# Kernel optimization log

Measured on AMD Instinct MI355X. Metric: run time of the kernel, lower is better.

The kernel has to match this reference:

```python
import jax, jax.numpy as jnp
import numpy as np

N = 50000
E = 800000
IN_C = 128
HID = 128
OUT_C = 64
HEADS = 8
HD1 = HID // HEADS   # 16 per-head dim, layer 1 (concat)
HD2 = OUT_C          # 64 per-head dim, layer 2 (concat=False, mean over heads)
NEG_SLOPE = 0.2


def setup_inputs() -> dict:
    key = jax.random.key(0)
    ks = jax.random.split(key, 12)
    x = jax.random.normal(ks[0], (N, IN_C), dtype=jnp.float32)
    edge_index = jax.random.randint(ks[1], (2, E), 0, N, dtype=jnp.int64)
    s1 = 1.0 / np.sqrt(IN_C)
    s2 = 1.0 / np.sqrt(HID)
    W1 = jax.random.normal(ks[2], (IN_C, HEADS * HD1), dtype=jnp.float32) * s1
    att_src1 = jax.random.normal(ks[3], (HEADS, HD1), dtype=jnp.float32) * s1
    att_dst1 = jax.random.normal(ks[4], (HEADS, HD1), dtype=jnp.float32) * s1
    b1 = jnp.zeros((HID,), dtype=jnp.float32)
    W2 = jax.random.normal(ks[5], (HID, HEADS * HD2), dtype=jnp.float32) * s2
    att_src2 = jax.random.normal(ks[6], (HEADS, HD2), dtype=jnp.float32) * s2
    att_dst2 = jax.random.normal(ks[7], (HEADS, HD2), dtype=jnp.float32) * s2
    b2 = jnp.zeros((OUT_C,), dtype=jnp.float32)
    return {"x": x, "edge_index": edge_index,
            "W1": W1, "att_src1": att_src1, "att_dst1": att_dst1, "b1": b1,
            "W2": W2, "att_src2": att_src2, "att_dst2": att_dst2, "b2": b2}


def _gat_conv(x, W, a_src, a_dst, bias, src, dst, heads, head_dim, concat):
    n = x.shape[0]
    h = (x @ W).reshape(n, heads, head_dim)                      # [N,H,D]
    alpha_s = jnp.einsum('nhd,hd->nh', h, a_src)                  # [N,H]
    alpha_d = jnp.einsum('nhd,hd->nh', h, a_dst)                  # [N,H]
    e = jax.nn.leaky_relu(alpha_s[src] + alpha_d[dst], NEG_SLOPE)  # [E,H]
    # segment softmax over edges grouped by destination node
    m = jax.ops.segment_max(e, dst, num_segments=n)               # [N,H]
    m = jnp.where(jnp.isfinite(m), m, 0.0)
    ex = jnp.exp(e - m[dst])
    denom = jax.ops.segment_sum(ex, dst, num_segments=n)
    alpha = ex / (denom[dst] + 1e-16)                             # [E,H]
    out = jax.ops.segment_sum(h[src] * alpha[:, :, None], dst, num_segments=n)  # [N,H,D]
    if concat:
        out = out.reshape(n, heads * head_dim)
    else:
        out = out.mean(axis=1)
    return out + bias


def reference(x, edge_index, W1, att_src1, att_dst1, b1, W2, att_src2, att_dst2, b2):
    # PyG GATConv default add_self_loops=True
    loops = jnp.arange(N, dtype=edge_index.dtype)
    src = jnp.concatenate([edge_index[0], loops])
    dst = jnp.concatenate([edge_index[1], loops])
    h = _gat_conv(x, W1, att_src1, att_dst1, b1, src, dst, HEADS, HD1, True)
    h = jax.nn.relu(h)
    out = _gat_conv(h, W2, att_src2, att_dst2, b2, src, dst, HEADS, HD2, False)
    return out
```

## Files before the change

kernel.cpp:

```cpp
#include <hip/hip_runtime.h>

#define N_NODES 50000
#define N_EDGES 800000
#define ET (N_EDGES + N_NODES)
#define HEADS 8
#define NPAD 50048
#define SCAN_NB 196
#define CAP 96

typedef __attribute__((ext_vector_type(8))) _Float16 half8;
typedef __attribute__((ext_vector_type(2))) _Float16 half2v;
typedef __attribute__((ext_vector_type(4))) float f32x4;

__device__ __forceinline__ int edge_src(const int* ei, int e, int is64){
  if (e >= N_EDGES) return e - N_EDGES;
  return is64 ? ei[2*e] : ei[e];
}
__device__ __forceinline__ int edge_dst(const int* ei, int e, int is64){
  if (e >= N_EDGES) return e - N_EDGES;
  return is64 ? ei[2*(N_EDGES + e)] : ei[N_EDGES + e];
}

__global__ void k_init(const int* __restrict__ ei, int* __restrict__ deg,
                       int* __restrict__ cnt, int* __restrict__ flag){
  int i = blockIdx.x*blockDim.x + threadIdx.x;
  if (i < N_NODES){ deg[i] = 0; cnt[i] = 0; }
  if (i == 0){
    int zeros = 0;
    for (int k = 0; k < 64; k++){
      if (ei[2*k + 1] == 0) zeros++;
    }
    *flag = (zeros >= 60) ? 1 : 0;
  }
}

__global__ void k_degree(const int* __restrict__ ei, int* __restrict__ deg,
                         const int* __restrict__ flag){
  int e = blockIdx.x*blockDim.x + threadIdx.x;
  if (e >= ET) return;
  int is64 = *flag;
  int d = edge_dst(ei, e, is64);
  atomicAdd(&deg[d], 1);
}

__global__ void k_scan_part(const int* __restrict__ deg, int* __restrict__ loc,
                            int* __restrict__ part){
  __shared__ int lds[256];
  int t = threadIdx.x, i = blockIdx.x*256 + t;
  int v = (i < N_NODES) ? deg[i] : 0;
  lds[t] = v;
  __syncthreads();
  for (int off = 1; off < 256; off <<= 1){
    int x = (t >= off) ? lds[t - off] : 0;
    __syncthreads();
    lds[t] += x;
    __syncthreads();
  }
  if (i < N_NODES) loc[i] = lds[t] - v;
  if (t == 255) part[blockIdx.x] = lds[255];
}

__global__ void k_scan_carry(int* __restrict__ part, int* __restrict__ carry){
  __shared__ int lds[256];
  int t = threadIdx.x;
  int v = (t < SCAN_NB) ? part[t] : 0;
  lds[t] = v;
  __syncthreads();
  for (int off = 1; off < 256; off <<= 1){
    int x = (t >= off) ? lds[t - off] : 0;
    __syncthreads();
    lds[t] += x;
    __syncthreads();
  }
  if (t < SCAN_NB) carry[t] = lds[t] - v;
}

__global__ void k_scan_add(const int* __restrict__ loc, const int* __restrict__ carry,
                           int* __restrict__ row_ptr){
  int i = blockIdx.x*blockDim.x + threadIdx.x;
  if (i < N_NODES) row_ptr[i] = loc[i] + carry[i >> 8];
  if (i == 0) row_ptr[N_NODES] = ET;
}

__global__ void k_fill(const int* __restrict__ ei, const int* __restrict__ row_ptr,
                       int* __restrict__ cnt, int* __restrict__ col,
                       const int* __restrict__ flag){
  int e = blockIdx.x*blockDim.x + threadIdx.x;
  if (e >= ET) return;
  int is64 = *flag;
  int s = edge_src(ei, e, is64);
  int d = edge_dst(ei, e, is64);
  int pos = atomicAdd(&cnt[d], 1);
  col[row_ptr[d] + pos] = s;
}

__global__ void k_wprep(const float* __restrict__ W1, const float* __restrict__ W2,
                        const float* __restrict__ as2, const float* __restrict__ ad2,
                        _Float16* __restrict__ Bp1, _Float16* __restrict__ Bp,
                        float* __restrict__ ws2, float* __restrict__ wd2){
  int b = blockIdx.x;
  int t_ = threadIdx.x;
  if (b < 256){
    int t = b*256 + t_;
    int j = t & 7, lane = (t >> 3) & 63, nt = (t >> 9) & 3, kt = t >> 11;
    int k = kt*32 + (lane >> 4)*8 + j;
    int c = nt*16 + (lane & 15);
    int h = k >> 7, kk = k & 127;
    Bp[t] = (_Float16)(0.125f * W2[kk*512 + h*64 + c]);
  } else if (b < 320){
    int t = (b - 256)*256 + t_;
    int j = t & 7, lane = (t >> 3) & 63, nt = (t >> 9) & 7, kt = t >> 12;
    int k = kt*32 + (lane >> 4)*8 + j;
    int c = nt*16 + (lane & 15);
    Bp1[t] = (_Float16)W1[k*128 + c];
  } else {
    int t = (b - 320)*256 + t_;
    int k = t >> 3, h = t & 7;
    float s = 0.f, d = 0.f;
    for (int dd = 0; dd < 64; dd++){
      float w = W2[k*512 + h*64 + dd];
      s += w * as2[h*64 + dd];
      d += w * ad2[h*64 + dd];
    }
    ws2[h*128 + k] = s;
    wd2[h*128 + k] = d;
  }
}

__global__ void __launch_bounds__(256) k_gemm1_mfma(
    const float* __restrict__ x, const _Float16* __restrict__ Bp1,
    _Float16* __restrict__ h1){
  int tid = threadIdx.x;
  int lane = tid & 63, wv = tid >> 6;
  int n0 = blockIdx.x*64 + wv*16;
  int rowA = n0 + (lane & 15);
  int koff = (lane >> 4)*8;
  const float* xr = x + (size_t)rowA*128 + koff;
  f32x4 acc[8];
  #pragma unroll
  for (int i = 0; i < 8; i++) acc[i] = (f32x4){0.f,0.f,0.f,0.f};
  bool inb = (rowA < N_NODES);
  #pragma unroll
  for (int kt = 0; kt < 4; kt++){
    half8 af;
    if (inb){
      float4 a0 = *(const float4*)(xr + kt*32);
      float4 a1 = *(const float4*)(xr + kt*32 + 4);
      af = (half8){(_Float16)a0.x,(_Float16)a0.y,(_Float16)a0.z,(_Float16)a0.w,
                   (_Float16)a1.x,(_Float16)a1.y,(_Float16)a1.z,(_Float16)a1.w};
    } else {
      af = (half8){0,0,0,0,0,0,0,0};
    }
    #pragma unroll
    for (int nt = 0; nt < 8; nt++){
      half8 bf = *(const half8*)(Bp1 + (((kt*8 + nt)*64 + lane) << 3));
      acc[nt] = __builtin_amdgcn_mfma_f32_16x16x32_f16(af, bf, acc[nt], 0, 0, 0);
    }
  }
  int r0 = n0 + (lane >> 4)*4;
  #pragma unroll
  for (int nt = 0; nt < 8; nt++){
    int c = nt*16 + (lane & 15);
    #pragma unroll
    for (int r = 0; r < 4; r++){
      int n = r0 + r;
      if (n < N_NODES) h1[(size_t)n*128 + c] = (_Float16)acc[nt][r];
    }
  }
}

__global__ void k_alpha1(const _Float16* __restrict__ h1, const float* __restrict__ as1,
                         const float* __restrict__ ad1,
                         float* __restrict__ als, float* __restrict__ ald){
  int t = blockIdx.x*blockDim.x + threadIdx.x;
  if (t >= N_NODES*8) return;
  int n = t >> 3, hh = t & 7;
  const half2v* hp = (const half2v*)(h1 + (size_t)n*128 + hh*16);
  float s = 0.f, d = 0.f;
  #pragma unroll
  for (int i = 0; i < 8; i++){
    half2v v = hp[i];
    float vx = (float)v.x, vy = (float)v.y;
    s += vx*as1[hh*16 + 2*i] + vy*as1[hh*16 + 2*i + 1];
    d += vx*ad1[hh*16 + 2*i] + vy*ad1[hh*16 + 2*i + 1];
  }
  als[t] = s; ald[t] = d;
}

__global__ void k_attn_agg1(const _Float16* __restrict__ h1,
    const float* __restrict__ als, const float* __restrict__ ald,
    const int* __restrict__ row_ptr, const int* __restrict__ col,
    const float* __restrict__ bias, _Float16* __restrict__ hr,
    const float* __restrict__ ws2, const float* __restrict__ wd2,
    float* __restrict__ als2, float* __restrict__ ald2){
  __shared__ _Float16 ew_s[4][CAP*8];
  __shared__ int col_s[4][CAP];
  int tid = threadIdx.x;
  int wv = tid >> 6, lane = tid & 63;
  int n = blockIdx.x*4 + wv;
  int beg = row_ptr[n], end = row_ptr[n+1];
  int deg = end - beg;
  int items = deg*8;
  int h = lane & 7;
  float ad = ald[n*8 + h];
  _Float16* es = ew_s[wv];
  int* cs = col_s[wv];
  float l = 0.f;
  for (int it = lane; it < items; it += 64){
    int e = it >> 3;
    int s = col[beg + e];
    float a = als[s*8 + h] + ad;
    a = (a > 0.f) ? a : 0.2f*a;
    float ex = __expf(a);
    if (it < CAP*8){
      es[it] = (_Float16)ex;
      if ((it & 7) == 0) cs[e] = s;
    }
    l += ex;
  }
  l += __shfl_xor(l, 8, 64);
  l += __shfl_xor(l, 16, 64);
  l += __shfl_xor(l, 32, 64);
  float inv = 1.f / (l + 1e-16f);
  __syncthreads();
  int hh0 = lane >> 3;
  float invh = __shfl(inv, hh0, 64);
  const half2v* h2p = (const half2v*)h1;
  float ax = 0.f, ay = 0.f;
  int degc = deg < CAP ? deg : CAP;
  int j = 0;
  for (; j + 3 < degc; j += 4){
    int s0 = cs[j], s1 = cs[j+1], s2 = cs[j+2], s3 = cs[j+3];
    float w0 = (float)es[j*8 + hh0]     * invh;
    float w1 = (float)es[(j+1)*8 + hh0] * invh;
    float w2 = (float)es[(j+2)*8 + hh0] * invh;
    float w3 = (float)es[(j+3)*8 + hh0] * invh;
    half2v v0 = h2p[(size_t)s0*64 + lane];
    half2v v1 = h2p[(size_t)s1*64 + lane];
    half2v v2 = h2p[(size_t)s2*64 + lane];
    half2v v3 = h2p[(size_t)s3*64 + lane];
    ax += w0*(float)v0.x + w1*(float)v1.x + w2*(float)v2.x + w3*(float)v3.x;
    ay += w0*(float)v0.y + w1*(float)v1.y + w2*(float)v2.y + w3*(float)v3.y;
  }
  for (; j < degc; j++){
    int s = cs[j];
    float w = (float)es[j*8 + hh0] * invh;
    half2v v = h2p[(size_t)s*64 + lane];
    ax += w*(float)v.x; ay += w*(float)v.y;
  }
  float adh = ald[n*8 + hh0];
  for (; j < deg; j++){
    int s = col[beg + j];
    float a = als[s*8 + hh0] + adh;
    a = (a > 0.f) ? a : 0.2f*a;
    float w = __expf(a)*invh;
    half2v v = h2p[(size_t)s*64 + lane];
    ax += w*(float)v.x; ay += w*(float)v.y;
  }
  float2 bb = ((const float2*)bias)[lane];
  float o0 = fmaxf(ax + bb.x, 0.f);
  float o1 = fmaxf(ay + bb.y, 0.f);
  half2v oo; oo.x = (_Float16)o0; oo.y = (_Float16)o1;
  ((half2v*)hr)[(size_t)n*64 + lane] = oo;
  const float2* wsp = (const float2*)ws2;
  const float2* wdp = (const float2*)wd2;
  #pragma unroll
  for (int hh = 0; hh < 8; hh++){
    float2 a = wsp[hh*64 + lane];
    float2 b = wdp[hh*64 + lane];
    float vs = o0*a.x + o1*a.y;
    float vd = o0*b.x + o1*b.y;
    #pragma unroll
    for (int off = 1; off < 64; off <<= 1){
      vs += __shfl_xor(vs, off, 64);
      vd += __shfl_xor(vd, off, 64);
    }
    if (lane == 0){
      als2[n*8 + hh] = vs;
      ald2[n*8 + hh] = vd;
    }
  }
}

__global__ void k_attn_agg2(const _Float16* __restrict__ hr,
    const float* __restrict__ als, const float* __restrict__ ald,
    const int* __restrict__ row_ptr, const int* __restrict__ col,
    _Float16* __restrict__ aggb){
  __shared__ _Float16 ew_s[4][CAP*8];
  __shared__ int col_s[4][CAP];
  int tid = threadIdx.x;
  int wv = tid >> 6, lane = tid & 63;
  int n = blockIdx.x*4 + wv;
  int beg = row_ptr[n], end = row_ptr[n+1];
  int deg = end - beg;
  int items = deg*8;
  int h = lane & 7;
  float ad = ald[n*8 + h];
  _Float16* es = ew_s[wv];
  int* cs = col_s[wv];
  float l = 0.f;
  for (int it = lane; it < items; it += 64){
    int e = it >> 3;
    int s = col[beg + e];
    float a = als[s*8 + h] + ad;
    a = (a > 0.f) ? a : 0.2f*a;
    float ex = __expf(a);
    if (it < CAP*8){
      es[it] = (_Float16)ex;
      if ((it & 7) == 0) cs[e] = s;
    }
    l += ex;
  }
  l += __shfl_xor(l, 8, 64);
  l += __shfl_xor(l, 16, 64);
  l += __shfl_xor(l, 32, 64);
  float inv = 1.f / (l + 1e-16f);
  __syncthreads();
  int hq = lane & 7, gq = lane >> 3;
  _Float16 inv16 = (_Float16)inv;
  half2v acc[8];
  #pragma unroll
  for (int i = 0; i < 8; i++) acc[i] = (half2v){(_Float16)0.f, (_Float16)0.f};
  int degc = deg < CAP ? deg : CAP;
  int j = 0;
  for (; j + 3 < degc; j += 4){
    int s0 = cs[j], s1 = cs[j+1], s2 = cs[j+2], s3 = cs[j+3];
    _Float16 w0 = es[j*8 + hq]     * inv16;
    _Float16 w1 = es[(j+1)*8 + hq] * inv16;
    _Float16 w2 = es[(j+2)*8 + hq] * inv16;
    _Float16 w3 = es[(j+3)*8 + hq] * inv16;
    half2v w0p = {w0, w0}, w1p = {w1, w1}, w2p = {w2, w2}, w3p = {w3, w3};
    const _Float16* p0 = hr + (size_t)s0*128 + gq*16;
    const _Float16* p1 = hr + (size_t)s1*128 + gq*16;
    const _Float16* p2 = hr + (size_t)s2*128 + gq*16;
    const _Float16* p3 = hr + (size_t)s3*128 + gq*16;
    half8 va0 = *(const half8*)p0, vb0 = *(const half8*)(p0 + 8);
    half8 va1 = *(const half8*)p1, vb1 = *(const half8*)(p1 + 8);
    half8 va2 = *(const half8*)p2, vb2 = *(const half8*)(p2 + 8);
    half8 va3 = *(const half8*)p3, vb3 = *(const half8*)(p3 + 8);
    #pragma unroll
    for (int k = 0; k < 4; k++){
      acc[k]   += w0p * (half2v){va0[2*k], va0[2*k+1]};
      acc[k+4] += w0p * (half2v){vb0[2*k], vb0[2*k+1]};
      acc[k]   += w1p * (half2v){va1[2*k], va1[2*k+1]};
      acc[k+4] += w1p * (half2v){vb1[2*k], vb1[2*k+1]};
      acc[k]   += w2p * (half2v){va2[2*k], va2[2*k+1]};
      acc[k+4] += w2p * (half2v){vb2[2*k], vb2[2*k+1]};
      acc[k]   += w3p * (half2v){va3[2*k], va3[2*k+1]};
      acc[k+4] += w3p * (half2v){vb3[2*k], vb3[2*k+1]};
    }
  }
  for (; j < degc; j++){
    int s = cs[j];
    _Float16 wh = es[j*8 + hq] * inv16;
    half2v wp = {wh, wh};
    const _Float16* p = hr + (size_t)s*128 + gq*16;
    half8 va = *(const half8*)p, vb = *(const half8*)(p + 8);
    #pragma unroll
    for (int k = 0; k < 4; k++){
      acc[k]   += wp * (half2v){va[2*k], va[2*k+1]};
      acc[k+4] += wp * (half2v){vb[2*k], vb[2*k+1]};
    }
  }
  for (; j < deg; j++){
    int s = col[beg + j];
    float a = als[s*8 + hq] + ad;
    a = (a > 0.f) ? a : 0.2f*a;
    _Float16 wh = (_Float16)(__expf(a)*inv);
    half2v wp = {wh, wh};
    const _Float16* p = hr + (size_t)s*128 + gq*16;
    half8 va = *(const half8*)p, vb = *(const half8*)(p + 8);
    #pragma unroll
    for (int k = 0; k < 4; k++){
      acc[k]   += wp * (half2v){va[2*k], va[2*k+1]};
      acc[k+4] += wp * (half2v){vb[2*k], vb[2*k+1]};
    }
  }
  _Float16* ar = aggb + (size_t)n*1024 + hq*128 + gq*16;
  half8 oa, ob;
  #pragma unroll
  for (int k = 0; k < 4; k++){
    oa[2*k] = acc[k].x;   oa[2*k+1] = acc[k].y;
    ob[2*k] = acc[k+4].x; ob[2*k+1] = acc[k+4].y;
  }
  *(half8*)ar = oa;
  *(half8*)(ar + 8) = ob;
}

__global__ void __launch_bounds__(256) k_gemm_out_mfma(
    const _Float16* __restrict__ aggb, const _Float16* __restrict__ Bp,
    const float* __restrict__ b2, float* __restrict__ outp){
  int tid = threadIdx.x;
  int lane = tid & 63, wv = tid >> 6;
  int n0 = blockIdx.x*64 + wv*16;
  int rowA = n0 + (lane & 15);
  const _Float16* arow = aggb + (size_t)rowA*1024 + (lane >> 4)*8;
  f32x4 acc[4];
  #pragma unroll
  for (int i = 0; i < 4; i++) acc[i] = (f32x4){0.f,0.f,0.f,0.f};
  half8 af = *(const half8*)(arow);
  for (int kt = 0; kt < 32; kt++){
    half8 afn;
    if (kt + 1 < 32) afn = *(const half8*)(arow + (kt+1)*32);
    #pragma unroll
    for (int nt = 0; nt < 4; nt++){
      half8 bf = *(const half8*)(Bp + (((kt*4 + nt)*64 + lane) << 3));
      acc[nt] = __builtin_amdgcn_mfma_f32_16x16x32_f16(af, bf, acc[nt], 0, 0, 0);
    }
    af = afn;
  }
  int r0 = n0 + (lane >> 4)*4;
  #pragma unroll
  for (int nt = 0; nt < 4; nt++){
    int c = nt*16 + (lane & 15);
    float bb = b2[c];
    #pragma unroll
    for (int r = 0; r < 4; r++){
      int n = r0 + r;
      if (n < N_NODES) outp[n*64 + c] = acc[nt][r] + bb;
    }
  }
}

extern "C" void kernel_launch(void* const* d_in, const int* in_sizes, int n_in,
                              void* d_out, int out_size, void* d_ws, size_t ws_size,
                              hipStream_t stream){
  const float* x   = (const float*)d_in[0];
  const int*   ei  = (const int*)d_in[1];
  const float* W1  = (const float*)d_in[2];
  const float* as1 = (const float*)d_in[3];
  const float* ad1 = (const float*)d_in[4];
  const float* b1  = (const float*)d_in[5];
  const float* W2  = (const float*)d_in[6];
  const float* as2 = (const float*)d_in[7];
  const float* ad2 = (const float*)d_in[8];
  const float* b2  = (const float*)d_in[9];
  float* outp = (float*)d_out;

  char* p = (char*)d_ws;
  auto alloc = [&](size_t bytes) -> void* {
    void* r = (void*)p;
    p += (bytes + 255) & ~(size_t)255;
    return r;
  };
  _Float16* aggb = (_Float16*)alloc((size_t)NPAD*1024*2);
  _Float16* h1  = aggb;
  _Float16* hr  = (_Float16*)alloc((size_t)N_NODES*128*2);
  float* als1 = (float*)alloc((size_t)N_NODES*8*4);
  float* ald1 = (float*)alloc((size_t)N_NODES*8*4);
  float* als2 = (float*)alloc((size_t)N_NODES*8*4);
  float* ald2 = (float*)alloc((size_t)N_NODES*8*4);
  int* row_ptr = (int*)alloc((size_t)(N_NODES+1)*4);
  int* deg  = (int*)alloc((size_t)N_NODES*4);
  int* cnt  = (int*)alloc((size_t)N_NODES*4);
  int* col  = (int*)alloc((size_t)ET*4);
  int* loc  = (int*)alloc((size_t)N_NODES*4);
  int* part = (int*)alloc(256*4);
  int* carry= (int*)alloc(256*4);
  int* flag = (int*)alloc(256);
  float* ws2 = (float*)alloc(1024*4);
  float* wd2 = (float*)alloc(1024*4);
  _Float16* Bp1 = (_Float16*)alloc((size_t)16384*2);
  _Float16* Bp  = (_Float16*)alloc((size_t)65536*2);

  dim3 b256(256);
  k_init<<<(N_NODES+255)/256, b256, 0, stream>>>(ei, deg, cnt, flag);
  k_degree<<<(ET+255)/256, b256, 0, stream>>>(ei, deg, flag);
  k_scan_part<<<SCAN_NB, b256, 0, stream>>>(deg, loc, part);
  k_scan_carry<<<1, b256, 0, stream>>>(part, carry);
  k_scan_add<<<SCAN_NB, b256, 0, stream>>>(loc, carry, row_ptr);
  k_fill<<<(ET+255)/256, b256, 0, stream>>>(ei, row_ptr, cnt, col, flag);
  k_wprep<<<324, b256, 0, stream>>>(W1, W2, as2, ad2, Bp1, Bp, ws2, wd2);

  int nnode_blocks = N_NODES/4;
  int nh_blocks = (N_NODES*8 + 255)/256;
  k_gemm1_mfma<<<NPAD/64, b256, 0, stream>>>(x, Bp1, h1);
  k_alpha1<<<nh_blocks, b256, 0, stream>>>(h1, as1, ad1, als1, ald1);
  k_attn_agg1<<<nnode_blocks, b256, 0, stream>>>(h1, als1, ald1, row_ptr, col,
                                                 b1, hr, ws2, wd2, als2, ald2);
  k_attn_agg2<<<nnode_blocks, b256, 0, stream>>>(hr, als2, ald2, row_ptr, col, aggb);
  k_gemm_out_mfma<<<NPAD/64, b256, 0, stream>>>(aggb, Bp, b2, outp);
}
```

Baseline: 384.6 us.

## Fuse alpha1 into GEMM1 epilogue and restructure layer-2 score reduction

```diff
diff --git a/kernel.cpp b/kernel.cpp
--- a/kernel.cpp
+++ b/kernel.cpp
@@ -129,7 +129,9 @@
 
 __global__ void __launch_bounds__(256) k_gemm1_mfma(
     const float* __restrict__ x, const _Float16* __restrict__ Bp1,
-    _Float16* __restrict__ h1){
+    _Float16* __restrict__ h1,
+    const float* __restrict__ as1, const float* __restrict__ ad1,
+    float* __restrict__ als1, float* __restrict__ ald1){
   int tid = threadIdx.x;
   int lane = tid & 63, wv = tid >> 6;
   int n0 = blockIdx.x*64 + wv*16;
@@ -157,34 +159,48 @@
       acc[nt] = __builtin_amdgcn_mfma_f32_16x16x32_f16(af, bf, acc[nt], 0, 0, 0);
     }
   }
-  int r0 = n0 + (lane >> 4)*4;
+  int m = lane & 15, q = lane >> 4;
+  int r0 = n0 + q*4;
   #pragma unroll
   for (int nt = 0; nt < 8; nt++){
-    int c = nt*16 + (lane & 15);
+    int c = nt*16 + m;
     #pragma unroll
     for (int r = 0; r < 4; r++){
       int n = r0 + r;
       if (n < N_NODES) h1[(size_t)n*128 + c] = (_Float16)acc[nt][r];
     }
   }
-}
-
-__global__ void k_alpha1(const _Float16* __restrict__ h1, const float* __restrict__ as1,
-                         const float* __restrict__ ad1,
-                         float* __restrict__ als, float* __restrict__ ald){
-  int t = blockIdx.x*blockDim.x + threadIdx.x;
-  if (t >= N_NODES*8) return;
-  int n = t >> 3, hh = t & 7;
-  const half2v* hp = (const half2v*)(h1 + (size_t)n*128 + hh*16);
-  float s = 0.f, d = 0.f;
-  #pragma unroll
-  for (int i = 0; i < 8; i++){
-    half2v v = hp[i];
-    float vx = (float)v.x, vy = (float)v.y;
-    s += vx*as1[hh*16 + 2*i] + vy*as1[hh*16 + 2*i + 1];
-    d += vx*ad1[hh*16 + 2*i] + vy*ad1[hh*16 + 2*i + 1];
-  }
-  als[t] = s; ald[t] = d;
+  float as1v[8], ad1v[8];
+  #pragma unroll
+  for (int nt = 0; nt < 8; nt++){
+    as1v[nt] = as1[nt*16 + m];
+    ad1v[nt] = ad1[nt*16 + m];
+  }
+  #pragma unroll
+  for (int r = 0; r < 4; r++){
+    float vs[8], vd[8];
+    #pragma unroll
+    for (int nt = 0; nt < 8; nt++){
+      vs[nt] = acc[nt][r]*as1v[nt];
+      vd[nt] = acc[nt][r]*ad1v[nt];
+      #pragma unroll
+      for (int off = 1; off < 16; off <<= 1){
+        vs[nt] += __shfl_xor(vs[nt], off, 64);
+        vd[nt] += __shfl_xor(vd[nt], off, 64);
+      }
+    }
+    int n = r0 + r;
+    if (m == r && n < N_NODES){
+      float4 v0; v0.x = vs[0]; v0.y = vs[1]; v0.z = vs[2]; v0.w = vs[3];
+      float4 v1; v1.x = vs[4]; v1.y = vs[5]; v1.z = vs[6]; v1.w = vs[7];
+      float4 w0; w0.x = vd[0]; w0.y = vd[1]; w0.z = vd[2]; w0.w = vd[3];
+      float4 w1; w1.x = vd[4]; w1.y = vd[5]; w1.z = vd[6]; w1.w = vd[7];
+      *(float4*)&als1[n*8]     = v0;
+      *(float4*)&als1[n*8 + 4] = v1;
+      *(float4*)&ald1[n*8]     = w0;
+      *(float4*)&ald1[n*8 + 4] = w1;
+    }
+  }
 }
 
 __global__ void k_attn_agg1(const _Float16* __restrict__ h1,
@@ -195,6 +211,7 @@
     float* __restrict__ als2, float* __restrict__ ald2){
   __shared__ _Float16 ew_s[4][CAP*8];
   __shared__ int col_s[4][CAP];
+  __shared__ _Float16 ot_s[4][132];
   int tid = threadIdx.x;
   int wv = tid >> 6, lane = tid & 63;
   int n = blockIdx.x*4 + wv;
@@ -206,17 +223,23 @@
   _Float16* es = ew_s[wv];
   int* cs = col_s[wv];
   float l = 0.f;
-  for (int it = lane; it < items; it += 64){
+  int itc = items < CAP*8 ? items : CAP*8;
+  int it = lane;
+  for (; it < itc; it += 64){
     int e = it >> 3;
     int s = col[beg + e];
     float a = als[s*8 + h] + ad;
     a = (a > 0.f) ? a : 0.2f*a;
     float ex = __expf(a);
-    if (it < CAP*8){
-      es[it] = (_Float16)ex;
-      if ((it & 7) == 0) cs[e] = s;
-    }
+    es[it] = (_Float16)ex;
+    if ((it & 7) == 0) cs[e] = s;
     l += ex;
+  }
+  for (; it < items; it += 64){
+    int s = col[beg + (it >> 3)];
+    float a = als[s*8 + h] + ad;
+    a = (a > 0.f) ? a : 0.2f*a;
+    l += __expf(a);
   }
   l += __shfl_xor(l, 8, 64);
   l += __shfl_xor(l, 16, 64);
@@ -229,18 +252,16 @@
   float ax = 0.f, ay = 0.f;
   int degc = deg < CAP ? deg : CAP;
   int j = 0;
-  for (; j + 3 < degc; j += 4){
-    int s0 = cs[j], s1 = cs[j+1], s2 = cs[j+2], s3 = cs[j+3];
-    float w0 = (float)es[j*8 + hh0]     * invh;
-    float w1 = (float)es[(j+1)*8 + hh0] * invh;
-    float w2 = (float)es[(j+2)*8 + hh0] * invh;
-    float w3 = (float)es[(j+3)*8 + hh0] * invh;
-    half2v v0 = h2p[(size_t)s0*64 + lane];
-    half2v v1 = h2p[(size_t)s1*64 + lane];
-    half2v v2 = h2p[(size_t)s2*64 + lane];
-    half2v v3 = h2p[(size_t)s3*64 + lane];
-    ax += w0*(float)v0.x + w1*(float)v1.x + w2*(float)v2.x + w3*(float)v3.x;
-    ay += w0*(float)v0.y + w1*(float)v1.y + w2*(float)v2.y + w3*(float)v3.y;
+  for (; j + 7 < degc; j += 8){
+    int s[8]; float w[8]; half2v v[8];
+    #pragma unroll
+    for (int u = 0; u < 8; u++) s[u] = cs[j + u];
+    #pragma unroll
+    for (int u = 0; u < 8; u++) w[u] = (float)es[(j + u)*8 + hh0] * invh;
+    #pragma unroll
+    for (int u = 0; u < 8; u++) v[u] = h2p[(size_t)s[u]*64 + lane];
+    #pragma unroll
+    for (int u = 0; u < 8; u++){ ax += w[u]*(float)v[u].x; ay += w[u]*(float)v[u].y; }
   }
   for (; j < degc; j++){
     int s = cs[j];
@@ -262,23 +283,25 @@
   float o1 = fmaxf(ay + bb.y, 0.f);
   half2v oo; oo.x = (_Float16)o0; oo.y = (_Float16)o1;
   ((half2v*)hr)[(size_t)n*64 + lane] = oo;
-  const float2* wsp = (const float2*)ws2;
-  const float2* wdp = (const float2*)wd2;
-  #pragma unroll
-  for (int hh = 0; hh < 8; hh++){
-    float2 a = wsp[hh*64 + lane];
-    float2 b = wdp[hh*64 + lane];
-    float vs = o0*a.x + o1*a.y;
-    float vd = o0*b.x + o1*b.y;
-    #pragma unroll
-    for (int off = 1; off < 64; off <<= 1){
-      vs += __shfl_xor(vs, off, 64);
-      vd += __shfl_xor(vd, off, 64);
-    }
-    if (lane == 0){
-      als2[n*8 + hh] = vs;
-      ald2[n*8 + hh] = vd;
-    }
+  ((half2v*)&ot_s[wv][0])[lane] = oo;
+  int hh = lane >> 3, seg = lane & 7;
+  const half2v* otp = (const half2v*)&ot_s[wv][0];
+  const float* wsr = ws2 + hh*128 + seg*16;
+  const float* wdr = wd2 + hh*128 + seg*16;
+  float vs = 0.f, vd = 0.f;
+  #pragma unroll
+  for (int i = 0; i < 8; i++){
+    half2v v = otp[seg*8 + i];
+    float vx = (float)v.x, vy = (float)v.y;
+    vs += vx*wsr[2*i] + vy*wsr[2*i + 1];
+    vd += vx*wdr[2*i] + vy*wdr[2*i + 1];
+  }
+  vs += __shfl_xor(vs, 1, 64); vd += __shfl_xor(vd, 1, 64);
+  vs += __shfl_xor(vs, 2, 64); vd += __shfl_xor(vd, 2, 64);
+  vs += __shfl_xor(vs, 4, 64); vd += __shfl_xor(vd, 4, 64);
+  if (seg == 0){
+    als2[n*8 + hh] = vs;
+    ald2[n*8 + hh] = vd;
   }
 }
 
@@ -299,17 +322,23 @@
   _Float16* es = ew_s[wv];
   int* cs = col_s[wv];
   float l = 0.f;
-  for (int it = lane; it < items; it += 64){
+  int itc = items < CAP*8 ? items : CAP*8;
+  int it = lane;
+  for (; it < itc; it += 64){
     int e = it >> 3;
     int s = col[beg + e];
     float a = als[s*8 + h] + ad;
     a = (a > 0.f) ? a : 0.2f*a;
     float ex = __expf(a);
-    if (it < CAP*8){
-      es[it] = (_Float16)ex;
-      if ((it & 7) == 0) cs[e] = s;
-    }
+    es[it] = (_Float16)ex;
+    if ((it & 7) == 0) cs[e] = s;
     l += ex;
+  }
+  for (; it < items; it += 64){
+    int s = col[beg + (it >> 3)];
+    float a = als[s*8 + h] + ad;
+    a = (a > 0.f) ? a : 0.2f*a;
+    l += __expf(a);
   }
   l += __shfl_xor(l, 8, 64);
   l += __shfl_xor(l, 16, 64);
@@ -473,9 +502,7 @@
   k_wprep<<<324, b256, 0, stream>>>(W1, W2, as2, ad2, Bp1, Bp, ws2, wd2);
 
   int nnode_blocks = N_NODES/4;
-  int nh_blocks = (N_NODES*8 + 255)/256;
-  k_gemm1_mfma<<<NPAD/64, b256, 0, stream>>>(x, Bp1, h1);
-  k_alpha1<<<nh_blocks, b256, 0, stream>>>(h1, as1, ad1, als1, ald1);
+  k_gemm1_mfma<<<NPAD/64, b256, 0, stream>>>(x, Bp1, h1, as1, ad1, als1, ald1);
   k_attn_agg1<<<nnode_blocks, b256, 0, stream>>>(h1, als1, ald1, row_ptr, col,
                                                  b1, hr, ws2, wd2, als2, ald2);
   k_attn_agg2<<<nnode_blocks, b256, 0, stream>>>(hr, als2, ald2, row_ptr, col, aggb);
```

Measured after the change: 375.0 us. -2.5%, faster.
